# Kernel tuning notes

Measured on AMD Instinct MI355X. Metric: run time of the kernel, lower is better.

The kernel has to match this reference:

```python
import jax, jax.numpy as jnp
import numpy as np

N_Q = 10           # qubits
N_BLOCKS = 10      # encoding blocks (== N_Q so adjoint start-index arithmetic matches source)
DIM = 1 << N_Q     # 1024 state-vector dimension
P = 128            # number of data points -> P*P pairwise circuit evaluations

SQRT2 = np.float32(np.sqrt(2.0))

# bits[d, q] = q-th bit (MSB-first) of basis index d
_bits_np = ((np.arange(DIM)[:, None] >> (N_Q - 1 - np.arange(N_Q))) & 1).astype(np.float32)
BITS = jnp.asarray(_bits_np)  # [DIM, N_Q]
# CRZ-ring diagonal feature: control q, target (q+1) % N_Q; phase exp(1j*theta_q*s_q*(s_{q+1}-1/2))
RING = jnp.asarray(_bits_np * (np.roll(_bits_np, -1, axis=1) - 0.5))  # [DIM, N_Q]


def _apply_1q(state, U, q):
    # state: [B, DIM]; apply 2x2 U to qubit q (MSB-first ordering)
    B = state.shape[0]
    s = state.reshape(B, 1 << q, 2, 1 << (N_Q - q - 1))
    s = jnp.einsum('ij,bajc->baic', U, s)
    return s.reshape(B, DIM)


def h_layer(state):
    H = jnp.asarray([[1, 1], [1, -1]], dtype=state.dtype) / SQRT2
    for q in range(N_Q):
        state = _apply_1q(state, H, q)
    return state


def rz_layer(state, thetas):
    # thetas: [B, N_Q] per-pair data angles; RZ(t) = diag(e^{-it/2}, e^{it/2})
    phases = jnp.exp(1j * jnp.einsum('dq,bq->bd', BITS - 0.5, thetas))
    return state * phases.astype(state.dtype)


def ry_layer(state, thetas):
    # thetas: [N_Q] shared trainable angles
    for q in range(N_Q):
        c, s = jnp.cos(thetas[q] / 2), jnp.sin(thetas[q] / 2)
        U = jnp.stack([jnp.stack([c, -s]), jnp.stack([s, c])]).astype(state.dtype)
        state = _apply_1q(state, U, q)
    return state


def crz_ring(state, thetas):
    # entire CRZ ring is diagonal in the computational basis -> single fused multiply
    phases = jnp.exp(1j * (RING @ thetas))  # [DIM]
    return state * phases.astype(state.dtype)


def circuit(x1, x2, params):
    # x1, x2: [B, N_BLOCKS*N_Q]; params: [N_BLOCKS, 2, N_Q]
    B = x1.shape[0]
    state = jnp.zeros((B, DIM), jnp.complex64).at[:, 0].set(1.0)
    for j in range(N_BLOCKS):  # block(...)
        state = h_layer(state)
        state = rz_layer(state, x1[:, j * N_Q:(j + 1) * N_Q])
        state = ry_layer(state, params[j, 0])
        state = crz_ring(state, params[j, 1])
    for k in range(N_BLOCKS):  # adj_block(...) over reversed(params)
        bp = params[N_BLOCKS - 1 - k]
        start = (N_Q - k - 1) * N_Q  # exactly as written in the source
        state = crz_ring(state, -bp[1])   # adjoint of diagonal gate = negated angles
        state = ry_layer(state, -bp[0])   # RY(-t); single-qubit gates commute across qubits
        state = rz_layer(state, -x2[:, start:start + N_Q])
        state = h_layer(state)            # H is self-adjoint
    return state


def setup_inputs() -> dict:
    key = jax.random.key(0)
    k1, k2, k3 = jax.random.split(key, 3)
    data = jax.random.normal(k1, (P, N_BLOCKS * N_Q), jnp.float32)
    labels = jnp.sign(jax.random.normal(k2, (P,), jnp.float32))  # +/-1 class labels
    params = jax.random.normal(k3, (N_BLOCKS, 2, N_Q), jnp.float32)
    return {"data": data, "labels": labels, "params": params}


def reference(data, labels, params):
    # k_fusion: kernel-target-alignment over all (i, j) pairs, fully batched
    n = data.shape[0]
    x1 = jnp.repeat(data, n, axis=0)   # point i for each pair (pair-major)
    x2 = jnp.tile(data, (n, 1))        # point j for each pair
    state = circuit(x1, x2, params)
    K = (jnp.abs(state[:, 0]) ** 2).reshape(n, n)  # probability of |0...0>
    ll = labels[:, None] * labels[None, :]
    polarity = jnp.sum(ll * K)
    norm = jnp.sqrt(jnp.sum(K ** 2) * jnp.sum(ll ** 2))
    return polarity / norm
```

## Files before the change

### kernel.cpp

```cpp
#include <hip/hip_runtime.h>
#include <math.h>

#define NQ   10
#define DIM  1024
#define NB   10
#define NPTS 128
#define S2   0.70710678118654752440f

#define TS 32
#define KC 64
#define KSPLIT (DIM / KC)
#define NBLK_RED 64

__device__ __forceinline__ void cmul_ph(float& vr, float& vi, float ph) {
    float s, c;
    __sincosf(ph, &s, &c);
    const float ar = vr, ai = vi;
    vr = ar * c - ai * s;
    vi = ar * s + ai * c;
}

#define H_PAIR(i0, i1) {                                   \
    const float ar = vr[i0], ai = vi[i0];                  \
    const float br = vr[i1], bi = vi[i1];                  \
    vr[i0] = (ar + br) * S2;  vi[i0] = (ai + bi) * S2;     \
    vr[i1] = (ar - br) * S2;  vi[i1] = (ai - bi) * S2; }

#define RY_PAIR(i0, i1, c, s) {                            \
    const float ar = vr[i0], ai = vi[i0];                  \
    const float br = vr[i1], bi = vi[i1];                  \
    vr[i0] = c * ar - s * br;  vi[i0] = c * ai - s * bi;   \
    vr[i1] = s * ar + c * br;  vi[i1] = s * ai + c * bi; }

__global__ __launch_bounds__(256)
void states_kernel(const float* __restrict__ data,
                   const float* __restrict__ params,
                   float2* __restrict__ psi,
                   double* __restrict__ acc,
                   int* __restrict__ cnt)
{
    __shared__ float aRe[DIM];
    __shared__ float aIm[DIM];
    __shared__ float bRe[DIM];
    __shared__ float bIm[DIM];

    const int tid  = threadIdx.x;
    const int w    = tid >> 6;
    const int lane = tid & 63;
    const int pt   = blockIdx.x;

    const int cbase = w * 256 + lane * 4;
    const int tb    = lane * 4 + w;

    if (pt == 0 && tid == 0) { acc[0] = 0.0; acc[1] = 0.0; cnt[0] = 0; }

    float vr[4], vi[4];
    vr[0] = vr[1] = vr[2] = vr[3] = 0.f;
    vi[0] = vi[1] = vi[2] = vi[3] = 0.f;
    if (tid == 0) vr[0] = 1.f;

    const float* x = data + pt * (NB * NQ);

    for (int j = 0; j < NB; ++j) {
        const float* ry  = params + j * 2 * NQ;
        const float* crz = ry + NQ;
        const float* xb  = x + j * NQ;

        H_PAIR(0, 2) H_PAIR(1, 3)
        H_PAIR(0, 1) H_PAIR(2, 3)
        #pragma unroll
        for (int l = 0; l < 6; ++l) {
            const float sg = ((lane >> l) & 1) ? -1.f : 1.f;
            #pragma unroll
            for (int r = 0; r < 4; ++r) {
                const float ur = __shfl_xor(vr[r], 1 << l, 64);
                const float ui = __shfl_xor(vi[r], 1 << l, 64);
                vr[r] = (ur + sg * vr[r]) * S2;
                vi[r] = (ui + sg * vi[r]) * S2;
            }
        }
        *(float4*)&aRe[cbase] = make_float4(vr[0], vr[1], vr[2], vr[3]);
        *(float4*)&aIm[cbase] = make_float4(vi[0], vi[1], vi[2], vi[3]);
        __syncthreads();
        #pragma unroll
        for (int k = 0; k < 4; ++k) { vr[k] = aRe[k * 256 + tb]; vi[k] = aIm[k * 256 + tb]; }
        H_PAIR(0, 2) H_PAIR(1, 3)
        H_PAIR(0, 1) H_PAIR(2, 3)

        {
            const float x0 = xb[0], x1 = xb[1];
            float base_ph = -0.5f * (x0 + x1);
            #pragma unroll
            for (int q = 2; q < NQ; ++q)
                base_ph += (((tb >> (9 - q)) & 1) - 0.5f) * xb[q];
            cmul_ph(vr[0], vi[0], base_ph);
            cmul_ph(vr[1], vi[1], base_ph + x1);
            cmul_ph(vr[2], vi[2], base_ph + x0);
            cmul_ph(vr[3], vi[3], base_ph + x0 + x1);
        }

        {
            float c, s;
            __sincosf(ry[0] * 0.5f, &s, &c);
            RY_PAIR(0, 2, c, s) RY_PAIR(1, 3, c, s)
            __sincosf(ry[1] * 0.5f, &s, &c);
            RY_PAIR(0, 1, c, s) RY_PAIR(2, 3, c, s)
        }
        #pragma unroll
        for (int l = 0; l < 6; ++l) {
            float c, s;
            __sincosf(ry[7 - l] * 0.5f, &s, &c);
            const float ss = ((lane >> l) & 1) ? s : -s;
            #pragma unroll
            for (int r = 0; r < 4; ++r) {
                const float ur = __shfl_xor(vr[r], 1 << l, 64);
                const float ui = __shfl_xor(vi[r], 1 << l, 64);
                vr[r] = c * vr[r] + ss * ur;
                vi[r] = c * vi[r] + ss * ui;
            }
        }
        #pragma unroll
        for (int k = 0; k < 4; ++k) { bRe[k * 256 + tb] = vr[k]; bIm[k * 256 + tb] = vi[k]; }
        __syncthreads();
        {
            const float4 fr = *(const float4*)&bRe[cbase];
            const float4 fi = *(const float4*)&bIm[cbase];
            vr[0] = fr.x; vr[1] = fr.y; vr[2] = fr.z; vr[3] = fr.w;
            vi[0] = fi.x; vi[1] = fi.y; vi[2] = fi.z; vi[3] = fi.w;
        }
        {
            float c, s;
            __sincosf(ry[8] * 0.5f, &s, &c);
            RY_PAIR(0, 2, c, s) RY_PAIR(1, 3, c, s)
            __sincosf(ry[9] * 0.5f, &s, &c);
            RY_PAIR(0, 1, c, s) RY_PAIR(2, 3, c, s)
        }

        {
            const int hb = (w << 6) | lane;
            float common = 0.f;
            #pragma unroll
            for (int q = 0; q <= 6; ++q) {
                const float bq  = (float)((hb >> (7 - q)) & 1);
                const float bq1 = (float)((hb >> (6 - q)) & 1);
                common += crz[q] * bq * (bq1 - 0.5f);
            }
            const float b2 = (float)(hb & 1);
            const float b9 = (float)((hb >> 7) & 1);
            const float t7 = crz[7], t8 = crz[8], t9 = crz[9];
            #pragma unroll
            for (int r = 0; r < 4; ++r) {
                const float r1 = (float)((r >> 1) & 1);
                const float r0 = (float)(r & 1);
                const float ph = common
                               + t7 * b2 * (r1 - 0.5f)
                               + t8 * r1 * (r0 - 0.5f)
                               + t9 * r0 * (b9 - 0.5f);
                cmul_ph(vr[r], vi[r], ph);
            }
        }
    }

    float2* out = psi + pt * DIM + cbase;
    *(float4*)&out[0] = make_float4(vr[0], vi[0], vr[1], vi[1]);
    *(float4*)&out[2] = make_float4(vr[2], vi[2], vr[3], vi[3]);
}

__global__ __launch_bounds__(256)
void gram_kernel(const float2* __restrict__ psi, float2* __restrict__ Gpart)
{
    __shared__ float2 A [TS][KC + 2];
    __shared__ float2 Bt[KC][TS + 2];

    const int tid  = threadIdx.x;
    const int bx   = blockIdx.x;
    const int ks   = bx & 15;
    const int tile = bx >> 4;
    const int ti   = tile >> 2, tj = tile & 3;
    const int kbase = ks * KC;

    #pragma unroll
    for (int it = 0; it < 2; ++it) {
        const int slot = it * 256 + tid;
        const int row  = slot >> 4;
        const int kq   = (slot & 15) << 2;
        const float4* sa = (const float4*)(psi + (ti * TS + row) * DIM + kbase + kq);
        const float4 a01 = sa[0], a23 = sa[1];
        *(float4*)&A[row][kq]     = a01;
        *(float4*)&A[row][kq + 2] = a23;
        const float4* sb = (const float4*)(psi + (tj * TS + row) * DIM + kbase + kq);
        const float4 b01 = sb[0], b23 = sb[1];
        Bt[kq + 0][row] = make_float2(b01.x, b01.y);
        Bt[kq + 1][row] = make_float2(b01.z, b01.w);
        Bt[kq + 2][row] = make_float2(b23.x, b23.y);
        Bt[kq + 3][row] = make_float2(b23.z, b23.w);
    }
    __syncthreads();

    const int ty = tid >> 4, tx = tid & 15;
    float g00r = 0.f, g00i = 0.f, g01r = 0.f, g01i = 0.f;
    float g10r = 0.f, g10i = 0.f, g11r = 0.f, g11i = 0.f;

    #pragma unroll 4
    for (int k = 0; k < KC; k += 2) {
        const float4 a0 = *(const float4*)&A[2 * ty    ][k];
        const float4 a1 = *(const float4*)&A[2 * ty + 1][k];
        const float4 b0 = *(const float4*)&Bt[k    ][2 * tx];
        const float4 b1 = *(const float4*)&Bt[k + 1][2 * tx];
        g00r += a0.x * b0.x + a0.y * b0.y;  g00i += a0.x * b0.y - a0.y * b0.x;
        g01r += a0.x * b0.z + a0.y * b0.w;  g01i += a0.x * b0.w - a0.y * b0.z;
        g10r += a1.x * b0.x + a1.y * b0.y;  g10i += a1.x * b0.y - a1.y * b0.x;
        g11r += a1.x * b0.z + a1.y * b0.w;  g11i += a1.x * b0.w - a1.y * b0.z;
        g00r += a0.z * b1.x + a0.w * b1.y;  g00i += a0.z * b1.y - a0.w * b1.x;
        g01r += a0.z * b1.z + a0.w * b1.w;  g01i += a0.z * b1.w - a0.w * b1.z;
        g10r += a1.z * b1.x + a1.w * b1.y;  g10i += a1.z * b1.y - a1.w * b1.x;
        g11r += a1.z * b1.z + a1.w * b1.w;  g11i += a1.z * b1.w - a1.w * b1.z;
    }

    float2* gp = Gpart + ks * (NPTS * NPTS);
    const int gr0 = ti * TS + 2 * ty, gc0 = tj * TS + 2 * tx;
    gp[(gr0    ) * NPTS + gc0    ] = make_float2(g00r, g00i);
    gp[(gr0    ) * NPTS + gc0 + 1] = make_float2(g01r, g01i);
    gp[(gr0 + 1) * NPTS + gc0    ] = make_float2(g10r, g10i);
    gp[(gr0 + 1) * NPTS + gc0 + 1] = make_float2(g11r, g11i);
}

__global__ __launch_bounds__(256)
void reduce_final(const float2* __restrict__ Gpart,
                  const float* __restrict__ labels,
                  double* __restrict__ acc,
                  int* __restrict__ cnt,
                  float* __restrict__ out)
{
    const int idx = blockIdx.x * 256 + threadIdx.x;
    float gr = 0.f, gi = 0.f;
    #pragma unroll
    for (int p = 0; p < KSPLIT; ++p) {
        const float2 g = Gpart[p * (NPTS * NPTS) + idx];
        gr += g.x; gi += g.y;
    }
    const int i  = idx >> 7;
    const int jj = idx & (NPTS - 1);
    const float K = gr * gr + gi * gi;
    double pol = (double)(labels[i] * labels[jj]) * (double)K;
    double k2  = (double)K * (double)K;
    #pragma unroll
    for (int off = 1; off < 64; off <<= 1) {
        pol += __shfl_xor(pol, off, 64);
        k2  += __shfl_xor(k2,  off, 64);
    }
    __shared__ double sp[4], sk[4];
    const int wv = threadIdx.x >> 6;
    if ((threadIdx.x & 63) == 0) { sp[wv] = pol; sk[wv] = k2; }
    __syncthreads();
    if (threadIdx.x == 0) {
        atomicAdd(&acc[0], sp[0] + sp[1] + sp[2] + sp[3]);
        atomicAdd(&acc[1], sk[0] + sk[1] + sk[2] + sk[3]);
        __threadfence();
        const int done = atomicAdd(cnt, 1);
        if (done == NBLK_RED - 1) {
            const double p  = atomicAdd(&acc[0], 0.0);
            const double s2 = atomicAdd(&acc[1], 0.0);
            double sumL2 = 0.0;
            for (int t = 0; t < NPTS; ++t) {
                const double l = (double)labels[t];
                sumL2 += l * l;
            }
            out[0] = (float)(p / (sumL2 * sqrt(s2)));
        }
    }
}

extern "C" void kernel_launch(void* const* d_in, const int* in_sizes, int n_in,
                              void* d_out, int out_size, void* d_ws, size_t ws_size,
                              hipStream_t stream)
{
    const float* data   = (const float*)d_in[0];
    const float* labels = (const float*)d_in[1];
    const float* params = (const float*)d_in[2];
    float* out = (float*)d_out;

    float2* psi   = (float2*)d_ws;
    float2* Gpart = (float2*)((char*)d_ws + (size_t)(1u << 20));
    double* acc   = (double*)((char*)d_ws + (size_t)(3u << 20));
    int*    cnt   = (int*)   ((char*)d_ws + (size_t)(3u << 20) + 16);

    states_kernel<<<NPTS, 256, 0, stream>>>(data, params, psi, acc, cnt);
    gram_kernel<<<256, 256, 0, stream>>>(psi, Gpart);
    reduce_final<<<NBLK_RED, 256, 0, stream>>>(Gpart, labels, acc, cnt, out);
}
```

Before: 96.32 us.

## Run state simulation with one wave per point and precomputed phase tables

```diff
diff --git a/kernel.cpp b/kernel.cpp
--- a/kernel.cpp
+++ b/kernel.cpp
@@ -12,9 +12,7 @@
 #define KSPLIT (DIM / KC)
 #define NBLK_RED 64
 
-__device__ __forceinline__ void cmul_ph(float& vr, float& vi, float ph) {
-    float s, c;
-    __sincosf(ph, &s, &c);
+__device__ __forceinline__ void cmul_cs(float& vr, float& vi, float c, float s) {
     const float ar = vr, ai = vi;
     vr = ar * c - ai * s;
     vi = ar * s + ai * c;
@@ -32,138 +30,198 @@
     vr[i0] = c * ar - s * br;  vi[i0] = c * ai - s * bi;   \
     vr[i1] = s * ar + c * br;  vi[i1] = s * ai + c * bi; }
 
-__global__ __launch_bounds__(256)
+__global__ __launch_bounds__(64)
 void states_kernel(const float* __restrict__ data,
                    const float* __restrict__ params,
                    float2* __restrict__ psi,
                    double* __restrict__ acc,
                    int* __restrict__ cnt)
 {
-    __shared__ float aRe[DIM];
-    __shared__ float aIm[DIM];
-    __shared__ float bRe[DIM];
-    __shared__ float bIm[DIM];
-
-    const int tid  = threadIdx.x;
-    const int w    = tid >> 6;
-    const int lane = tid & 63;
+    __shared__ __align__(16) float Tre[64 * 20];
+    __shared__ __align__(16) float Tim[64 * 20];
+    __shared__ float  sX  [NB * NQ];
+    __shared__ float  sRyC[NB * NQ];
+    __shared__ float  sRyS[NB * NQ];
+    __shared__ float  sCrz[NB * NQ];
+    __shared__ float  sBase[NB];
+    __shared__ float2 sRz[NB * 16];
+    __shared__ float2 sRc[NB * 4 * 17];
+
+    const int lane = threadIdx.x;
     const int pt   = blockIdx.x;
 
-    const int cbase = w * 256 + lane * 4;
-    const int tb    = lane * 4 + w;
-
-    if (pt == 0 && tid == 0) { acc[0] = 0.0; acc[1] = 0.0; cnt[0] = 0; }
-
-    float vr[4], vi[4];
-    vr[0] = vr[1] = vr[2] = vr[3] = 0.f;
-    vi[0] = vi[1] = vi[2] = vi[3] = 0.f;
-    if (tid == 0) vr[0] = 1.f;
-
-    const float* x = data + pt * (NB * NQ);
+    if (pt == 0 && lane == 0) { acc[0] = 0.0; acc[1] = 0.0; cnt[0] = 0; }
+
+    for (int i = lane; i < NB * NQ; i += 64) {
+        sX[i] = data[pt * (NB * NQ) + i];
+        const int j = i / NQ, q = i - j * NQ;
+        float s, c;
+        __sincosf(0.5f * params[j * 2 * NQ + q], &s, &c);
+        sRyC[i] = c; sRyS[i] = s;
+        sCrz[i] = params[j * 2 * NQ + NQ + q];
+    }
+    if (lane < NB) {
+        float s = 0.f;
+        #pragma unroll
+        for (int q = 0; q < NQ; ++q) s += sX[lane * NQ + q];
+        sBase[lane] = -0.5f * s;
+    }
+    for (int e = lane; e < NB * 16; e += 64) {
+        const int j = e >> 4, m = e & 15;
+        float T = 0.f;
+        #pragma unroll
+        for (int q = 0; q < 4; ++q)
+            T += (float)((m >> (3 - q)) & 1) * sX[j * NQ + q];
+        float s, c;
+        __sincosf(T, &s, &c);
+        sRz[e] = make_float2(c, s);
+    }
+    for (int e = lane; e < NB * 64; e += 64) {
+        const int j = e >> 6, r = e & 63, bc = r >> 4, m = r & 15;
+        const float b4 = (float)((bc >> 1) & 1);
+        const float b9 = (float)(bc & 1);
+        const float m3 = (float)((m >> 3) & 1), m2 = (float)((m >> 2) & 1);
+        const float m1 = (float)((m >> 1) & 1), m0 = (float)(m & 1);
+        const float g = sCrz[j * NQ + 5] * b4 * (m3 - 0.5f)
+                      + sCrz[j * NQ + 6] * m3 * (m2 - 0.5f)
+                      + sCrz[j * NQ + 7] * m2 * (m1 - 0.5f)
+                      + sCrz[j * NQ + 8] * m1 * (m0 - 0.5f)
+                      + sCrz[j * NQ + 9] * m0 * (b9 - 0.5f);
+        float s, c;
+        __sincosf(g, &s, &c);
+        sRc[(j * 4 + bc) * 17 + m] = make_float2(c, s);
+    }
+
+    float vr[16], vi[16];
+    #pragma unroll
+    for (int m = 0; m < 16; ++m) { vr[m] = 0.f; vi[m] = 0.f; }
+    if (lane == 0) vr[0] = 1.f;
+
+    const int trow = (lane >> 4) * 20 + (lane & 15);
 
     for (int j = 0; j < NB; ++j) {
-        const float* ry  = params + j * 2 * NQ;
-        const float* crz = ry + NQ;
-        const float* xb  = x + j * NQ;
-
-        H_PAIR(0, 2) H_PAIR(1, 3)
-        H_PAIR(0, 1) H_PAIR(2, 3)
-        #pragma unroll
-        for (int l = 0; l < 6; ++l) {
+        const int j10 = j * NQ;
+
+        #pragma unroll
+        for (int b = 3; b >= 0; --b) {
+            const int bit = 1 << b;
+            #pragma unroll
+            for (int m = 0; m < 16; ++m)
+                if (!(m & bit)) { H_PAIR(m, m | bit) }
+        }
+        #pragma unroll
+        for (int l = 0; l < 2; ++l) {
             const float sg = ((lane >> l) & 1) ? -1.f : 1.f;
             #pragma unroll
-            for (int r = 0; r < 4; ++r) {
-                const float ur = __shfl_xor(vr[r], 1 << l, 64);
-                const float ui = __shfl_xor(vi[r], 1 << l, 64);
-                vr[r] = (ur + sg * vr[r]) * S2;
-                vi[r] = (ui + sg * vi[r]) * S2;
-            }
-        }
-        *(float4*)&aRe[cbase] = make_float4(vr[0], vr[1], vr[2], vr[3]);
-        *(float4*)&aIm[cbase] = make_float4(vi[0], vi[1], vi[2], vi[3]);
-        __syncthreads();
-        #pragma unroll
-        for (int k = 0; k < 4; ++k) { vr[k] = aRe[k * 256 + tb]; vi[k] = aIm[k * 256 + tb]; }
-        H_PAIR(0, 2) H_PAIR(1, 3)
-        H_PAIR(0, 1) H_PAIR(2, 3)
+            for (int m = 0; m < 16; ++m) {
+                const float ur = __shfl_xor(vr[m], 1 << l, 64);
+                const float ui = __shfl_xor(vi[m], 1 << l, 64);
+                vr[m] = (ur + sg * vr[m]) * S2;
+                vi[m] = (ui + sg * vi[m]) * S2;
+            }
+        }
+        #pragma unroll
+        for (int k = 0; k < 4; ++k) {
+            *(float4*)&Tre[lane * 20 + 4 * k] = make_float4(vr[4*k], vr[4*k+1], vr[4*k+2], vr[4*k+3]);
+            *(float4*)&Tim[lane * 20 + 4 * k] = make_float4(vi[4*k], vi[4*k+1], vi[4*k+2], vi[4*k+3]);
+        }
+        #pragma unroll
+        for (int m = 0; m < 16; ++m) {
+            vr[m] = Tre[m * 80 + trow];
+            vi[m] = Tim[m * 80 + trow];
+        }
+        #pragma unroll
+        for (int b = 3; b >= 0; --b) {
+            const int bit = 1 << b;
+            #pragma unroll
+            for (int m = 0; m < 16; ++m)
+                if (!(m & bit)) { H_PAIR(m, m | bit) }
+        }
 
         {
-            const float x0 = xb[0], x1 = xb[1];
-            float base_ph = -0.5f * (x0 + x1);
-            #pragma unroll
-            for (int q = 2; q < NQ; ++q)
-                base_ph += (((tb >> (9 - q)) & 1) - 0.5f) * xb[q];
-            cmul_ph(vr[0], vi[0], base_ph);
-            cmul_ph(vr[1], vi[1], base_ph + x1);
-            cmul_ph(vr[2], vi[2], base_ph + x0);
-            cmul_ph(vr[3], vi[3], base_ph + x0 + x1);
+            float lp = sBase[j];
+            #pragma unroll
+            for (int q = 4; q < NQ; ++q)
+                lp = fmaf((float)((lane >> (9 - q)) & 1), sX[j10 + q], lp);
+            float sl, cl;
+            __sincosf(lp, &sl, &cl);
+            #pragma unroll
+            for (int m = 0; m < 16; ++m) {
+                const float2 z = sRz[j * 16 + m];
+                const float rc = cl * z.x - sl * z.y;
+                const float rs = cl * z.y + sl * z.x;
+                cmul_cs(vr[m], vi[m], rc, rs);
+            }
+        }
+
+        #pragma unroll
+        for (int q = 0; q < 4; ++q) {
+            const float c = sRyC[j10 + q], s = sRyS[j10 + q];
+            const int bit = 1 << (3 - q);
+            #pragma unroll
+            for (int m = 0; m < 16; ++m)
+                if (!(m & bit)) { RY_PAIR(m, m | bit, c, s) }
+        }
+        #pragma unroll
+        for (int m = 0; m < 16; ++m) {
+            Tre[m * 80 + trow] = vr[m];
+            Tim[m * 80 + trow] = vi[m];
+        }
+        #pragma unroll
+        for (int k = 0; k < 4; ++k) {
+            const float4 fr = *(const float4*)&Tre[lane * 20 + 4 * k];
+            const float4 fi = *(const float4*)&Tim[lane * 20 + 4 * k];
+            vr[4*k] = fr.x; vr[4*k+1] = fr.y; vr[4*k+2] = fr.z; vr[4*k+3] = fr.w;
+            vi[4*k] = fi.x; vi[4*k+1] = fi.y; vi[4*k+2] = fi.z; vi[4*k+3] = fi.w;
+        }
+        #pragma unroll
+        for (int q = 6; q < 10; ++q) {
+            const float c = sRyC[j10 + q], s = sRyS[j10 + q];
+            const int bit = 1 << (9 - q);
+            #pragma unroll
+            for (int m = 0; m < 16; ++m)
+                if (!(m & bit)) { RY_PAIR(m, m | bit, c, s) }
+        }
+        #pragma unroll
+        for (int l = 0; l < 2; ++l) {
+            const float c = sRyC[j10 + 5 - l];
+            const float s = sRyS[j10 + 5 - l];
+            const float ss = ((lane >> l) & 1) ? s : -s;
+            #pragma unroll
+            for (int m = 0; m < 16; ++m) {
+                const float ur = __shfl_xor(vr[m], 1 << l, 64);
+                const float ui = __shfl_xor(vi[m], 1 << l, 64);
+                vr[m] = c * vr[m] + ss * ur;
+                vi[m] = c * vi[m] + ss * ui;
+            }
         }
 
         {
-            float c, s;
-            __sincosf(ry[0] * 0.5f, &s, &c);
-            RY_PAIR(0, 2, c, s) RY_PAIR(1, 3, c, s)
-            __sincosf(ry[1] * 0.5f, &s, &c);
-            RY_PAIR(0, 1, c, s) RY_PAIR(2, 3, c, s)
-        }
-        #pragma unroll
-        for (int l = 0; l < 6; ++l) {
-            float c, s;
-            __sincosf(ry[7 - l] * 0.5f, &s, &c);
-            const float ss = ((lane >> l) & 1) ? s : -s;
-            #pragma unroll
-            for (int r = 0; r < 4; ++r) {
-                const float ur = __shfl_xor(vr[r], 1 << l, 64);
-                const float ui = __shfl_xor(vi[r], 1 << l, 64);
-                vr[r] = c * vr[r] + ss * ur;
-                vi[r] = c * vi[r] + ss * ui;
-            }
-        }
-        #pragma unroll
-        for (int k = 0; k < 4; ++k) { bRe[k * 256 + tb] = vr[k]; bIm[k * 256 + tb] = vi[k]; }
-        __syncthreads();
-        {
-            const float4 fr = *(const float4*)&bRe[cbase];
-            const float4 fi = *(const float4*)&bIm[cbase];
-            vr[0] = fr.x; vr[1] = fr.y; vr[2] = fr.z; vr[3] = fr.w;
-            vi[0] = fi.x; vi[1] = fi.y; vi[2] = fi.z; vi[3] = fi.w;
-        }
-        {
-            float c, s;
-            __sincosf(ry[8] * 0.5f, &s, &c);
-            RY_PAIR(0, 2, c, s) RY_PAIR(1, 3, c, s)
-            __sincosf(ry[9] * 0.5f, &s, &c);
-            RY_PAIR(0, 1, c, s) RY_PAIR(2, 3, c, s)
-        }
-
-        {
-            const int hb = (w << 6) | lane;
-            float common = 0.f;
-            #pragma unroll
-            for (int q = 0; q <= 6; ++q) {
-                const float bq  = (float)((hb >> (7 - q)) & 1);
-                const float bq1 = (float)((hb >> (6 - q)) & 1);
-                common += crz[q] * bq * (bq1 - 0.5f);
-            }
-            const float b2 = (float)(hb & 1);
-            const float b9 = (float)((hb >> 7) & 1);
-            const float t7 = crz[7], t8 = crz[8], t9 = crz[9];
-            #pragma unroll
-            for (int r = 0; r < 4; ++r) {
-                const float r1 = (float)((r >> 1) & 1);
-                const float r0 = (float)(r & 1);
-                const float ph = common
-                               + t7 * b2 * (r1 - 0.5f)
-                               + t8 * r1 * (r0 - 0.5f)
-                               + t9 * r0 * (b9 - 0.5f);
-                cmul_ph(vr[r], vi[r], ph);
-            }
-        }
-    }
-
-    float2* out = psi + pt * DIM + cbase;
-    *(float4*)&out[0] = make_float4(vr[0], vi[0], vr[1], vi[1]);
-    *(float4*)&out[2] = make_float4(vr[2], vi[2], vr[3], vi[3]);
+            float cm = 0.f;
+            #pragma unroll
+            for (int q = 0; q <= 4; ++q) {
+                const float bc_ = (float)((lane >> (5 - q)) & 1);
+                const float bt_ = (float)((lane >> (4 - q)) & 1);
+                cm += sCrz[j10 + q] * bc_ * (bt_ - 0.5f);
+            }
+            float sc, cc;
+            __sincosf(cm, &sc, &cc);
+            const int bc = ((lane & 1) << 1) | ((lane >> 5) & 1);
+            const float2* __restrict__ rcp = &sRc[(j * 4 + bc) * 17];
+            #pragma unroll
+            for (int m = 0; m < 16; ++m) {
+                const float2 z = rcp[m];
+                const float rr = cc * z.x - sc * z.y;
+                const float ri = cc * z.y + sc * z.x;
+                cmul_cs(vr[m], vi[m], rr, ri);
+            }
+        }
+    }
+
+    float2* o = psi + (size_t)pt * DIM + lane * 16;
+    #pragma unroll
+    for (int k = 0; k < 8; ++k)
+        *(float4*)&o[2 * k] = make_float4(vr[2*k], vi[2*k], vr[2*k+1], vi[2*k+1]);
 }
 
 __global__ __launch_bounds__(256)
@@ -285,7 +343,7 @@
     double* acc   = (double*)((char*)d_ws + (size_t)(3u << 20));
     int*    cnt   = (int*)   ((char*)d_ws + (size_t)(3u << 20) + 16);
 
-    states_kernel<<<NPTS, 256, 0, stream>>>(data, params, psi, acc, cnt);
+    states_kernel<<<NPTS, 64, 0, stream>>>(data, params, psi, acc, cnt);
     gram_kernel<<<256, 256, 0, stream>>>(psi, Gpart);
     reduce_final<<<NBLK_RED, 256, 0, stream>>>(Gpart, labels, acc, cnt, out);
 }
```

New measurement: 108.9 us. 13.1% more time.

## Fuse H, RZ and RY per qubit into precomputed 2x2 unitaries with ping-pong layout

Applied to the files above, without the earlier changes.

```diff
diff --git a/kernel.cpp b/kernel.cpp
--- a/kernel.cpp
+++ b/kernel.cpp
@@ -12,25 +12,11 @@
 #define KSPLIT (DIM / KC)
 #define NBLK_RED 64
 
-__device__ __forceinline__ void cmul_ph(float& vr, float& vi, float ph) {
-    float s, c;
-    __sincosf(ph, &s, &c);
-    const float ar = vr, ai = vi;
-    vr = ar * c - ai * s;
-    vi = ar * s + ai * c;
-}
-
-#define H_PAIR(i0, i1) {                                   \
-    const float ar = vr[i0], ai = vi[i0];                  \
-    const float br = vr[i1], bi = vi[i1];                  \
-    vr[i0] = (ar + br) * S2;  vi[i0] = (ai + bi) * S2;     \
-    vr[i1] = (ar - br) * S2;  vi[i1] = (ai - bi) * S2; }
-
-#define RY_PAIR(i0, i1, c, s) {                            \
-    const float ar = vr[i0], ai = vi[i0];                  \
-    const float br = vr[i1], bi = vi[i1];                  \
-    vr[i0] = c * ar - s * br;  vi[i0] = c * ai - s * bi;   \
-    vr[i1] = s * ar + c * br;  vi[i1] = s * ai + c * bi; }
+typedef float f2 __attribute__((ext_vector_type(2)));
+
+__device__ __forceinline__ f2 cmul(f2 a, f2 b) {
+    return (f2){a.x * b.x - a.y * b.y, a.x * b.y + a.y * b.x};
+}
 
 __global__ __launch_bounds__(256)
 void states_kernel(const float* __restrict__ data,
@@ -39,131 +25,138 @@
                    double* __restrict__ acc,
                    int* __restrict__ cnt)
 {
-    __shared__ float aRe[DIM];
-    __shared__ float aIm[DIM];
-    __shared__ float bRe[DIM];
-    __shared__ float bIm[DIM];
+    __shared__ f2    Tb[2][16 * 64];
+    __shared__ f2    UT[NB * NQ * 4];
+    __shared__ float sCrz[NB * NQ];
 
     const int tid  = threadIdx.x;
     const int w    = tid >> 6;
     const int lane = tid & 63;
     const int pt   = blockIdx.x;
 
-    const int cbase = w * 256 + lane * 4;
-    const int tb    = lane * 4 + w;
-
     if (pt == 0 && tid == 0) { acc[0] = 0.0; acc[1] = 0.0; cnt[0] = 0; }
 
-    float vr[4], vi[4];
-    vr[0] = vr[1] = vr[2] = vr[3] = 0.f;
-    vi[0] = vi[1] = vi[2] = vi[3] = 0.f;
-    if (tid == 0) vr[0] = 1.f;
-
-    const float* x = data + pt * (NB * NQ);
-
-    for (int j = 0; j < NB; ++j) {
-        const float* ry  = params + j * 2 * NQ;
-        const float* crz = ry + NQ;
-        const float* xb  = x + j * NQ;
-
-        H_PAIR(0, 2) H_PAIR(1, 3)
-        H_PAIR(0, 1) H_PAIR(2, 3)
-        #pragma unroll
-        for (int l = 0; l < 6; ++l) {
-            const float sg = ((lane >> l) & 1) ? -1.f : 1.f;
-            #pragma unroll
-            for (int r = 0; r < 4; ++r) {
-                const float ur = __shfl_xor(vr[r], 1 << l, 64);
-                const float ui = __shfl_xor(vi[r], 1 << l, 64);
-                vr[r] = (ur + sg * vr[r]) * S2;
-                vi[r] = (ui + sg * vi[r]) * S2;
-            }
-        }
-        *(float4*)&aRe[cbase] = make_float4(vr[0], vr[1], vr[2], vr[3]);
-        *(float4*)&aIm[cbase] = make_float4(vi[0], vi[1], vi[2], vi[3]);
-        __syncthreads();
-        #pragma unroll
-        for (int k = 0; k < 4; ++k) { vr[k] = aRe[k * 256 + tb]; vi[k] = aIm[k * 256 + tb]; }
-        H_PAIR(0, 2) H_PAIR(1, 3)
-        H_PAIR(0, 1) H_PAIR(2, 3)
-
-        {
-            const float x0 = xb[0], x1 = xb[1];
-            float base_ph = -0.5f * (x0 + x1);
-            #pragma unroll
-            for (int q = 2; q < NQ; ++q)
-                base_ph += (((tb >> (9 - q)) & 1) - 0.5f) * xb[q];
-            cmul_ph(vr[0], vi[0], base_ph);
-            cmul_ph(vr[1], vi[1], base_ph + x1);
-            cmul_ph(vr[2], vi[2], base_ph + x0);
-            cmul_ph(vr[3], vi[3], base_ph + x0 + x1);
-        }
-
-        {
-            float c, s;
-            __sincosf(ry[0] * 0.5f, &s, &c);
-            RY_PAIR(0, 2, c, s) RY_PAIR(1, 3, c, s)
-            __sincosf(ry[1] * 0.5f, &s, &c);
-            RY_PAIR(0, 1, c, s) RY_PAIR(2, 3, c, s)
-        }
-        #pragma unroll
-        for (int l = 0; l < 6; ++l) {
-            float c, s;
-            __sincosf(ry[7 - l] * 0.5f, &s, &c);
-            const float ss = ((lane >> l) & 1) ? s : -s;
-            #pragma unroll
-            for (int r = 0; r < 4; ++r) {
-                const float ur = __shfl_xor(vr[r], 1 << l, 64);
-                const float ui = __shfl_xor(vi[r], 1 << l, 64);
-                vr[r] = c * vr[r] + ss * ur;
-                vi[r] = c * vi[r] + ss * ui;
-            }
-        }
-        #pragma unroll
-        for (int k = 0; k < 4; ++k) { bRe[k * 256 + tb] = vr[k]; bIm[k * 256 + tb] = vi[k]; }
-        __syncthreads();
-        {
-            const float4 fr = *(const float4*)&bRe[cbase];
-            const float4 fi = *(const float4*)&bIm[cbase];
-            vr[0] = fr.x; vr[1] = fr.y; vr[2] = fr.z; vr[3] = fr.w;
-            vi[0] = fi.x; vi[1] = fi.y; vi[2] = fi.z; vi[3] = fi.w;
-        }
-        {
-            float c, s;
-            __sincosf(ry[8] * 0.5f, &s, &c);
-            RY_PAIR(0, 2, c, s) RY_PAIR(1, 3, c, s)
-            __sincosf(ry[9] * 0.5f, &s, &c);
-            RY_PAIR(0, 1, c, s) RY_PAIR(2, 3, c, s)
-        }
-
-        {
-            const int hb = (w << 6) | lane;
-            float common = 0.f;
-            #pragma unroll
-            for (int q = 0; q <= 6; ++q) {
-                const float bq  = (float)((hb >> (7 - q)) & 1);
-                const float bq1 = (float)((hb >> (6 - q)) & 1);
-                common += crz[q] * bq * (bq1 - 0.5f);
-            }
-            const float b2 = (float)(hb & 1);
-            const float b9 = (float)((hb >> 7) & 1);
-            const float t7 = crz[7], t8 = crz[8], t9 = crz[9];
-            #pragma unroll
-            for (int r = 0; r < 4; ++r) {
-                const float r1 = (float)((r >> 1) & 1);
-                const float r0 = (float)(r & 1);
-                const float ph = common
-                               + t7 * b2 * (r1 - 0.5f)
-                               + t8 * r1 * (r0 - 0.5f)
-                               + t9 * r0 * (b9 - 0.5f);
-                cmul_ph(vr[r], vi[r], ph);
-            }
-        }
-    }
-
-    float2* out = psi + pt * DIM + cbase;
-    *(float4*)&out[0] = make_float4(vr[0], vi[0], vr[1], vi[1]);
-    *(float4*)&out[2] = make_float4(vr[2], vi[2], vr[3], vi[3]);
+    if (tid < NB * NQ) {
+        const int j = tid / NQ, q = tid - j * NQ;
+        const float th = params[j * 2 * NQ + q];
+        float c, s;
+        __sincosf(0.5f * th, &s, &c);
+        const float x = data[pt * (NB * NQ) + tid];
+        float cx, sx;
+        __sincosf(0.5f * x, &sx, &cx);
+        const float al = (c - s) * S2, be = (c + s) * S2;
+        f2* u = &UT[tid * 4];
+        u[0] = (f2){ al * cx, -be * sx};
+        u[1] = (f2){ be * cx, -al * sx};
+        u[2] = (f2){ be * cx,  al * sx};
+        u[3] = (f2){-al * cx, -be * sx};
+        sCrz[tid] = params[j * 2 * NQ + NQ + q];
+    }
+    __syncthreads();
+
+    f2 v[4];
+    #pragma unroll
+    for (int m = 0; m < 4; ++m) v[m] = (f2){0.f, 0.f};
+    if (tid == 0) v[0] = (f2){1.f, 0.f};
+
+    const float B2 = (float)( lane       & 1), B3 = (float)((lane >> 1) & 1);
+    const float B4 = (float)((lane >> 2) & 1), B5 = (float)((lane >> 3) & 1);
+    const float B6 = (float)((lane >> 4) & 1), B7 = (float)((lane >> 5) & 1);
+
+    #define LOAD_U(j, q) \
+        const f2* _u = &UT[((j) * NQ + (q)) * 4]; \
+        const f2 u0 = _u[0], u1 = _u[1], u2 = _u[2], u3 = _u[3];
+
+    #define APPLY_LOCAL(j, q, bit) { \
+        LOAD_U(j, q) \
+        _Pragma("unroll") \
+        for (int m = 0; m < 4; ++m) if (!(m & (bit))) { \
+            const f2 a0 = v[m], a1 = v[m | (bit)]; \
+            v[m]         = cmul(u0, a0) + cmul(u1, a1); \
+            v[m | (bit)] = cmul(u2, a0) + cmul(u3, a1); \
+        } }
+
+    #define APPLY_SHUFFLE(j, q, mb) { \
+        LOAD_U(j, q) \
+        const bool hi = lane & (mb); \
+        const f2 cv = hi ? u3 : u0; \
+        const f2 cp = hi ? u2 : u1; \
+        _Pragma("unroll") \
+        for (int m = 0; m < 4; ++m) { \
+            const f2 p = { __shfl_xor(v[m].x, (mb), 64), \
+                           __shfl_xor(v[m].y, (mb), 64) }; \
+            v[m] = cmul(cv, v[m]) + cmul(cp, p); \
+        } }
+
+    #define TRANSPOSE(buf) { \
+        f2* T = Tb[buf]; \
+        _Pragma("unroll") \
+        for (int m = 0; m < 4; ++m) T[(w * 4 + m) * 64 + lane] = v[m]; \
+        __syncthreads(); \
+        f2 nv0 = T[(0 * 4 + w) * 64 + lane]; \
+        f2 nv1 = T[(1 * 4 + w) * 64 + lane]; \
+        f2 nv2 = T[(2 * 4 + w) * 64 + lane]; \
+        f2 nv3 = T[(3 * 4 + w) * 64 + lane]; \
+        v[0] = nv0; v[1] = nv1; v[2] = nv2; v[3] = nv3; }
+
+    #define APPLY_CRZ(j, hiIsAmp) { \
+        const float* phi = &sCrz[(j) * NQ]; \
+        const float laneOnly = phi[2] * B7 * (B6 - 0.5f) \
+                             + phi[3] * B6 * (B5 - 0.5f) \
+                             + phi[4] * B5 * (B4 - 0.5f) \
+                             + phi[5] * B4 * (B3 - 0.5f) \
+                             + phi[6] * B3 * (B2 - 0.5f); \
+        _Pragma("unroll") \
+        for (int m = 0; m < 4; ++m) { \
+            const int hi2 = (hiIsAmp) ? m : w; \
+            const int lo2 = (hiIsAmp) ? w : m; \
+            const float b9 = (float)((hi2 >> 1) & 1), b8 = (float)(hi2 & 1); \
+            const float b1 = (float)((lo2 >> 1) & 1), b0 = (float)(lo2 & 1); \
+            const float ph = laneOnly \
+                           + phi[0] * b9 * (b8 - 0.5f) \
+                           + phi[1] * b8 * (B7 - 0.5f) \
+                           + phi[7] * B2 * (b1 - 0.5f) \
+                           + phi[8] * b1 * (b0 - 0.5f) \
+                           + phi[9] * b0 * (b9 - 0.5f); \
+            float sc, cc; \
+            __sincosf(ph, &sc, &cc); \
+            v[m] = cmul(v[m], (f2){cc, sc}); \
+        } }
+
+    #pragma unroll
+    for (int jj = 0; jj < NB / 2; ++jj) {
+        const int je = 2 * jj;
+        APPLY_LOCAL(je, 9, 1)
+        APPLY_LOCAL(je, 8, 2)
+        APPLY_SHUFFLE(je, 7, 1)
+        APPLY_SHUFFLE(je, 6, 2)
+        APPLY_SHUFFLE(je, 5, 4)
+        APPLY_SHUFFLE(je, 4, 8)
+        APPLY_SHUFFLE(je, 3, 16)
+        APPLY_SHUFFLE(je, 2, 32)
+        TRANSPOSE(0)
+        APPLY_LOCAL(je, 1, 1)
+        APPLY_LOCAL(je, 0, 2)
+        APPLY_CRZ(je, true)
+
+        const int jo = je + 1;
+        APPLY_LOCAL(jo, 1, 1)
+        APPLY_LOCAL(jo, 0, 2)
+        APPLY_SHUFFLE(jo, 7, 1)
+        APPLY_SHUFFLE(jo, 6, 2)
+        APPLY_SHUFFLE(jo, 5, 4)
+        APPLY_SHUFFLE(jo, 4, 8)
+        APPLY_SHUFFLE(jo, 3, 16)
+        APPLY_SHUFFLE(jo, 2, 32)
+        TRANSPOSE(1)
+        APPLY_LOCAL(jo, 9, 1)
+        APPLY_LOCAL(jo, 8, 2)
+        APPLY_CRZ(jo, false)
+    }
+
+    float2* o = psi + (size_t)pt * DIM + w * 256 + lane * 4;
+    *(float4*)&o[0] = make_float4(v[0].x, v[0].y, v[1].x, v[1].y);
+    *(float4*)&o[2] = make_float4(v[2].x, v[2].y, v[3].x, v[3].y);
 }
 
 __global__ __launch_bounds__(256)
```

New measurement: 88.42 us. 8.2% less time.
